# Optimization experiments

Measured on AMD Instinct MI355X. Metric: run time of the kernel, lower is better.

The kernel has to match this reference:

```python
import jax, jax.numpy as jnp
import numpy as np

B, N, C, H = 4, 2048, 1024, 16
D = C // H  # head_dim = 64
SCALE = D ** -0.5


def setup_inputs() -> dict:
    key = jax.random.key(0)
    ks = jax.random.split(key, 7)
    # freqs_cis = exp(i*theta): unit-modulus rotations, as in standard RoPE
    theta = jax.random.uniform(ks[1], (B, N, D // 2), jnp.float32, 0.0, 2 * np.pi)
    return {
        "x": jax.random.normal(ks[0], (B, N, C), jnp.float32),
        "freqs_cos": jnp.cos(theta),
        "freqs_sin": jnp.sin(theta),
        "attn_mask": jax.random.normal(ks[2], (1, 1, N, N), jnp.float32) * 0.1,
        "Wqkv": jax.random.normal(ks[3], (3 * C, C), jnp.float32) * (C ** -0.5),
        "Wproj": jax.random.normal(ks[4], (C, C), jnp.float32) * (C ** -0.5),
        "bproj": jnp.zeros((C,), jnp.float32),
    }


def _rope(t, cos, sin):
    # t: [B,H,N,D]; cos/sin: [B,1,N,D/2]; complex multiply on interleaved pairs
    tr = t.reshape(*t.shape[:-1], D // 2, 2)
    t0, t1 = tr[..., 0], tr[..., 1]
    out = jnp.stack([t0 * cos - t1 * sin, t0 * sin + t1 * cos], axis=-1)
    return out.reshape(t.shape)


def reference(x, freqs_cos, freqs_sin, attn_mask, Wqkv, Wproj, bproj):
    qkv = x @ Wqkv.T  # [B,N,3C]
    qkv = qkv.reshape(B, N, 3, H, D).transpose(2, 0, 3, 1, 4)  # [3,B,H,N,D]
    q, k, v = qkv[0], qkv[1], qkv[2]
    cos = freqs_cos[:, None]  # [B,1,N,D/2]
    sin = freqs_sin[:, None]
    q = _rope(q, cos, sin)
    k = _rope(k, cos, sin)
    attn = jnp.einsum("bhnd,bhmd->bhnm", q * SCALE, k) + attn_mask
    attn = jax.nn.softmax(attn, axis=-1)
    out = jnp.einsum("bhnm,bhmd->bhnd", attn, v)  # [B,H,N,D]
    out = out.transpose(0, 2, 1, 3).reshape(B, N, C)
    return out @ Wproj.T + bproj
```

## Files before the change

kernel.cpp:

```cpp
#include <hip/hip_runtime.h>
#include <hip/hip_bf16.h>
#include <stdint.h>


typedef __bf16 bf16;
typedef __bf16 bf16x4 __attribute__((ext_vector_type(4)));
typedef __bf16 bf16x8 __attribute__((ext_vector_type(8)));
typedef float  f32x4  __attribute__((ext_vector_type(4)));
typedef float  f32x16 __attribute__((ext_vector_type(16)));
typedef int    int4v  __attribute__((ext_vector_type(4)));

#define MFMA16(a, b, c) __builtin_amdgcn_mfma_f32_16x16x32_bf16((a), (b), (c), 0, 0, 0)
#define MFMA32(a, b, c) __builtin_amdgcn_mfma_f32_32x32x16_bf16((a), (b), (c), 0, 0, 0)

__device__ __forceinline__ bf16x4 cvt4s(float a, float b, float c, float d) {
  bf16x4 r;
  r[0] = (bf16)a; r[1] = (bf16)b; r[2] = (bf16)c; r[3] = (bf16)d;
  return r;
}
__device__ __forceinline__ bf16x8 cvt8(f32x4 a, f32x4 b) {
  bf16x8 r;
  r[0] = (bf16)a[0]; r[1] = (bf16)a[1]; r[2] = (bf16)a[2]; r[3] = (bf16)a[3];
  r[4] = (bf16)b[0]; r[5] = (bf16)b[1]; r[6] = (bf16)b[2]; r[7] = (bf16)b[3];
  return r;
}

template<int MODE>
__global__ __launch_bounds__(256)
void gemm_bt(const void* __restrict__ Av, const float* __restrict__ B,
             void* __restrict__ O0, bf16* __restrict__ O1, bf16* __restrict__ O2,
             const float* __restrict__ bias)
{
  constexpr int K = 1024;
  __shared__ __attribute__((aligned(16))) bf16 As[128 * 64];
  __shared__ __attribute__((aligned(16))) bf16 Bs[128 * 64];
  const int tid = threadIdx.x, lane = tid & 63, wid = tid >> 6;
  const int m0 = blockIdx.x * 128, n0 = blockIdx.y * 128;
  const int wm = (wid >> 1) * 64, wn = (wid & 1) * 64;
  const int l15 = lane & 15, lg = lane >> 4;

  f32x4 acc[4][4] = {};

  for (int k0 = 0; k0 < K; k0 += 64) {
#pragma unroll
    for (int it = 0; it < 4; ++it) {
      const int e = (it * 256 + tid) * 8;
      const int row = e >> 6, col = e & 63;
      const float* bp = B + (size_t)(n0 + row) * K + k0 + col;
      *(bf16x8*)(Bs + row * 64 + col) =
          cvt8(*(const f32x4*)bp, *(const f32x4*)(bp + 4));
    }
    if (MODE == 0) {
      const float* A = (const float*)Av;
#pragma unroll
      for (int it = 0; it < 4; ++it) {
        const int e = (it * 256 + tid) * 8;
        const int row = e >> 6, col = e & 63;
        const float* ap = A + (size_t)(m0 + row) * K + k0 + col;
        *(bf16x8*)(As + row * 64 + col) =
            cvt8(*(const f32x4*)ap, *(const f32x4*)(ap + 4));
      }
    } else {
      const bf16* A = (const bf16*)Av;
#pragma unroll
      for (int it = 0; it < 4; ++it) {
        const int e = (it * 256 + tid) * 8;
        const int row = e >> 6, col = e & 63;
        *(bf16x8*)(As + row * 64 + col) =
            *(const bf16x8*)(A + (size_t)(m0 + row) * K + k0 + col);
      }
    }
    __syncthreads();

    bf16x8 af[4][2], bb[4][2];
#pragma unroll
    for (int i = 0; i < 4; ++i)
#pragma unroll
      for (int kk = 0; kk < 2; ++kk) {
        af[i][kk] = *(const bf16x8*)(As + (wm + i * 16 + l15) * 64 + kk * 32 + lg * 8);
        bb[i][kk] = *(const bf16x8*)(Bs + (wn + i * 16 + l15) * 64 + kk * 32 + lg * 8);
      }
#pragma unroll
    for (int mi = 0; mi < 4; ++mi)
#pragma unroll
      for (int ni = 0; ni < 4; ++ni)
#pragma unroll
        for (int kk = 0; kk < 2; ++kk)
          acc[mi][ni] = MFMA16(af[mi][kk], bb[ni][kk], acc[mi][ni]);
    __syncthreads();
  }

#pragma unroll
  for (int mi = 0; mi < 4; ++mi)
#pragma unroll
    for (int ni = 0; ni < 4; ++ni)
#pragma unroll
      for (int r = 0; r < 4; ++r) {
        const int row = m0 + wm + mi * 16 + lg * 4 + r;
        const int col = n0 + wn + ni * 16 + l15;
        float v = acc[mi][ni][r];
        if (MODE == 0) {
          const int s = col >> 10, h = (col >> 6) & 15, d = col & 63;
          const int b = row >> 11, n = row & 2047;
          const bf16 bv = (bf16)v;
          if (s == 0)
            ((bf16*)O0)[(((size_t)(b * 16 + h) * 2048) + n) * 64 + d] = bv;
          else if (s == 1)
            O1[(((size_t)(b * 16 + h) * 2048) + n) * 64 + d] = bv;
          else
            O2[(((size_t)(b * 16 + h) * 64) + d) * 2048 + n] = bv;
        } else {
          ((float*)O0)[(size_t)row * 1024 + col] = v + bias[col];
        }
      }
}

__global__ __launch_bounds__(256)
void rope_k(bf16* __restrict__ Q, bf16* __restrict__ K,
            const float* __restrict__ C, const float* __restrict__ S)
{
  const int gid = blockIdx.x * 256 + threadIdx.x;
  const int part = gid & 3;
  const int rowid = gid >> 2;
  const int n = rowid & 2047;
  const int b = rowid >> 15;
  const size_t cbase = ((size_t)(b * 2048 + n)) * 32 + part * 8;

  float cf[8], sf[8];
  *(f32x4*)cf = *(const f32x4*)(C + cbase);
  *(f32x4*)(cf + 4) = *(const f32x4*)(C + cbase + 4);
  *(f32x4*)sf = *(const f32x4*)(S + cbase);
  *(f32x4*)(sf + 4) = *(const f32x4*)(S + cbase + 4);

  bf16* qp = Q + (size_t)rowid * 64 + part * 16;
  bf16* kp = K + (size_t)rowid * 64 + part * 16;
  __attribute__((aligned(16))) bf16 buf[16];

  *(int4v*)buf = *(const int4v*)qp;
  *(int4v*)(buf + 8) = *(const int4v*)(qp + 8);
#pragma unroll
  for (int j = 0; j < 8; ++j) {
    const float t0 = (float)buf[2 * j], t1 = (float)buf[2 * j + 1];
    buf[2 * j]     = (bf16)(t0 * cf[j] - t1 * sf[j]);
    buf[2 * j + 1] = (bf16)(t0 * sf[j] + t1 * cf[j]);
  }
  *(int4v*)qp = *(int4v*)buf;
  *(int4v*)(qp + 8) = *(int4v*)(buf + 8);

  *(int4v*)buf = *(const int4v*)kp;
  *(int4v*)(buf + 8) = *(const int4v*)(kp + 8);
#pragma unroll
  for (int j = 0; j < 8; ++j) {
    const float t0 = (float)buf[2 * j], t1 = (float)buf[2 * j + 1];
    buf[2 * j]     = (bf16)(t0 * cf[j] - t1 * sf[j]);
    buf[2 * j + 1] = (bf16)(t0 * sf[j] + t1 * cf[j]);
  }
  *(int4v*)kp = *(int4v*)buf;
  *(int4v*)(kp + 8) = *(int4v*)(buf + 8);
}

__global__ __launch_bounds__(256, 4)
void attn_k(const bf16* __restrict__ Q, const bf16* __restrict__ K,
            const bf16* __restrict__ VT, const float* __restrict__ M,
             bf16* __restrict__ O)
{
  constexpr float SCALE_LOG2E = 0.125f * 1.4426950408889634f;
  constexpr float LOG2E = 1.4426950408889634f;
  __shared__ __attribute__((aligned(16))) bf16 SH[9216];
  bf16* Kt = SH;
  bf16* Vt = SH + 4096;

  const int tid = threadIdx.x, lane = tid & 63, w = tid >> 6;
  const int bh = blockIdx.x;
  const int q0 = blockIdx.y * 128;
  const int b = bh >> 4, h = bh & 15;
  const int l31 = lane & 31, hi = lane >> 5;
  const int swz = (l31 & 7) << 3;

  const bf16* Qb = Q + (size_t)bh * 2048 * 64;
  const bf16* Kb = K + (size_t)bh * 2048 * 64;
  const bf16* Vb = VT + (size_t)bh * 64 * 2048;
  const float* Mq = M + (size_t)(q0 + w * 32 + l31) * 2048;

  bf16x8 qf[4];
  {
    const bf16* qr = Qb + (size_t)(q0 + w * 32 + l31) * 64 + 8 * hi;
#pragma unroll
    for (int j = 0; j < 4; ++j) qf[j] = *(const bf16x8*)(qr + 16 * j);
  }

  f32x16 o[2] = {{0,0,0,0,0,0,0,0,0,0,0,0,0,0,0,0},
                 {0,0,0,0,0,0,0,0,0,0,0,0,0,0,0,0}};
  float li = 0.f;

  for (int kv0 = 0; kv0 < 2048; kv0 += 64) {
#pragma unroll
    for (int it = 0; it < 2; ++it) {
      const int idx = it * 256 + tid;
      const int row = idx >> 3, g8 = (idx & 7) * 8;
      const int sc = g8 ^ ((row & 7) << 3);
      *(int4v*)(Kt + row * 64 + sc) =
          *(const int4v*)(Kb + (size_t)(kv0 + row) * 64 + g8);
      *(int4v*)(Vt + row * 64 + sc) =
          *(const int4v*)(Vb + (size_t)row * 2048 + kv0 + g8);
    }

    f32x4 mk_all[2][4];
#pragma unroll
    for (int sub = 0; sub < 2; ++sub)
#pragma unroll
      for (int rg = 0; rg < 4; ++rg)
        mk_all[sub][rg] = *(const f32x4*)(Mq + kv0 + 32 * sub + 8 * rg + 4 * hi);

    __syncthreads();

#pragma unroll
    for (int sub = 0; sub < 2; ++sub) {
      f32x16 s = {0,0,0,0,0,0,0,0,0,0,0,0,0,0,0,0};
#pragma unroll
      for (int j = 0; j < 4; ++j) {
        const bf16x8 kf = *(const bf16x8*)(
            Kt + (sub * 32 + l31) * 64 + ((16 * j + 8 * hi) ^ swz));
        s = MFMA32(kf, qf[j], s);
      }

      float rs = 0.f;
#pragma unroll
      for (int rg = 0; rg < 4; ++rg)
#pragma unroll
        for (int i = 0; i < 4; ++i) {
          const float p = __builtin_exp2f(
              fmaf(s[4 * rg + i], SCALE_LOG2E, mk_all[sub][rg][i] * LOG2E));
          s[4 * rg + i] = p;
          rs += p;
        }
      rs += __shfl_xor(rs, 32);
      li += rs;

      uint32_t pk0, pk1, pk2, pk3, pk4, pk5, pk6, pk7;
      asm("v_cvt_pk_bf16_f32 %0, %1, %2" : "=v"(pk0) : "v"(s[0]),  "v"(s[1]));
      asm("v_cvt_pk_bf16_f32 %0, %1, %2" : "=v"(pk1) : "v"(s[2]),  "v"(s[3]));
      asm("v_cvt_pk_bf16_f32 %0, %1, %2" : "=v"(pk2) : "v"(s[4]),  "v"(s[5]));
      asm("v_cvt_pk_bf16_f32 %0, %1, %2" : "=v"(pk3) : "v"(s[6]),  "v"(s[7]));
      asm("v_cvt_pk_bf16_f32 %0, %1, %2" : "=v"(pk4) : "v"(s[8]),  "v"(s[9]));
      asm("v_cvt_pk_bf16_f32 %0, %1, %2" : "=v"(pk5) : "v"(s[10]), "v"(s[11]));
      asm("v_cvt_pk_bf16_f32 %0, %1, %2" : "=v"(pk6) : "v"(s[12]), "v"(s[13]));
      asm("v_cvt_pk_bf16_f32 %0, %1, %2" : "=v"(pk7) : "v"(s[14]), "v"(s[15]));
      asm("v_permlane32_swap_b32 %0, %1" : "+v"(pk0), "+v"(pk2));
      asm("v_permlane32_swap_b32 %0, %1" : "+v"(pk1), "+v"(pk3));
      asm("v_permlane32_swap_b32 %0, %1" : "+v"(pk4), "+v"(pk6));
      asm("v_permlane32_swap_b32 %0, %1" : "+v"(pk5), "+v"(pk7));
      uint32_t pau[2][4] = {{pk0, pk1, pk2, pk3}, {pk4, pk5, pk6, pk7}};
      bf16x8 pa[2];
      __builtin_memcpy(&pa[0], pau[0], 16);
      __builtin_memcpy(&pa[1], pau[1], 16);

#pragma unroll
      for (int kh = 0; kh < 2; ++kh)
#pragma unroll
        for (int dblk = 0; dblk < 2; ++dblk) {
          const bf16x8 vf = *(const bf16x8*)(
              Vt + (dblk * 32 + l31) * 64 + ((sub * 32 + kh * 16 + 8 * hi) ^ swz));
          o[dblk] = MFMA32(vf, pa[kh], o[dblk]);
        }
    }
    __syncthreads();
  }

  const float inv = 1.f / li;
  bf16* ow = SH + w * 2304;
#pragma unroll
  for (int dblk = 0; dblk < 2; ++dblk)
#pragma unroll
    for (int rg = 0; rg < 4; ++rg)
      *(bf16x4*)(ow + l31 * 72 + dblk * 32 + 8 * rg + 4 * hi) =
          cvt4s(o[dblk][4 * rg] * inv, o[dblk][4 * rg + 1] * inv,
                o[dblk][4 * rg + 2] * inv, o[dblk][4 * rg + 3] * inv);
  asm volatile("s_waitcnt lgkmcnt(0)" ::: "memory");
  __builtin_amdgcn_sched_barrier(0);
#pragma unroll
  for (int p = 0; p < 4; ++p) {
    const int row = p * 8 + (lane >> 3);
    const int n = q0 + w * 32 + row;
    const int4v v = *(const int4v*)(ow + row * 72 + (lane & 7) * 8);
    *(int4v*)(O + ((size_t)b * 2048 + n) * 1024 + h * 64 + (lane & 7) * 8) = v;
  }
}

extern "C" void kernel_launch(void* const* d_in, const int* in_sizes, int n_in,
                              void* d_out, int out_size, void* d_ws, size_t ws_size,
                              hipStream_t stream)
{
  (void)in_sizes; (void)n_in; (void)out_size;
  const float* x     = (const float*)d_in[0];
  const float* fcos  = (const float*)d_in[1];
  const float* fsin  = (const float*)d_in[2];
  const float* mask  = (const float*)d_in[3];
  const float* wqkv  = (const float*)d_in[4];
  const float* wproj = (const float*)d_in[5];
  const float* bproj = (const float*)d_in[6];
  float* out = (float*)d_out;

  const size_t SZ = (size_t)64 * 2048 * 64 * 2;
  if (ws_size < 4 * SZ) return;
  char* ws = (char*)d_ws;
  bf16* Qr = (bf16*)(ws);
  bf16* Kr = (bf16*)(ws + SZ);
  bf16* VT = (bf16*)(ws + 2 * SZ);
  bf16* Ob = (bf16*)(ws + 3 * SZ);

  gemm_bt<0><<<dim3(64, 24), 256, 0, stream>>>(x, wqkv, Qr, Kr, VT, nullptr);
  rope_k<<<2048, 256, 0, stream>>>(Qr, Kr, fcos, fsin);
  attn_k<<<dim3(64, 16), 256, 0, stream>>>(Qr, Kr, VT, mask, Ob);
  gemm_bt<1><<<dim3(64, 8), 256, 0, stream>>>(Ob, wproj, out, nullptr, nullptr, bproj);
}
```

Before: 320.7 us.

## Pre-convert weights and mask to bf16, use direct-to-LDS loads, add MFMA priority

Adds a conversion kernel that turns Wqkv, Wproj and the attention mask (pre-scaled by log2e) into bf16 buffers in the workspace before the GEMMs and attention run. The GEMM B operand, and the A operand in the bf16 mode, are then loaded with global_load_lds straight into shared memory instead of being converted per tile in registers. Attention reads the bf16 mask, halving the mask traffic each block repeats, and wraps its MFMA sections in s_setprio. The cost is extra conversion launches and workspace use, with a fallback to the fp32 mask path when the workspace is too small.

```diff
diff --git a/kernel.cpp b/kernel.cpp
--- a/kernel.cpp
+++ b/kernel.cpp
@@ -24,10 +24,24 @@
   r[4] = (bf16)b[0]; r[5] = (bf16)b[1]; r[6] = (bf16)b[2]; r[7] = (bf16)b[3];
   return r;
 }
+__device__ __forceinline__ void gload16(const void* g, void* l) {
+  __builtin_amdgcn_global_load_lds((const __attribute__((address_space(1))) void*)g,
+                                   (__attribute__((address_space(3))) void*)l, 16, 0, 0);
+}
+
+__global__ __launch_bounds__(256)
+void cvt_k(const float* __restrict__ W, bf16* __restrict__ Wb, float scale)
+{
+  const size_t i = ((size_t)blockIdx.x * 256 + threadIdx.x) * 8;
+  const float* p = W + i;
+  f32x4 a = *(const f32x4*)p * scale;
+  f32x4 b = *(const f32x4*)(p + 4) * scale;
+  *(bf16x8*)(Wb + i) = cvt8(a, b);
+}
 
 template<int MODE>
 __global__ __launch_bounds__(256)
-void gemm_bt(const void* __restrict__ Av, const float* __restrict__ B,
+void gemm_bt(const void* __restrict__ Av, const bf16* __restrict__ B,
              void* __restrict__ O0, bf16* __restrict__ O1, bf16* __restrict__ O2,
              const float* __restrict__ bias)
 {
@@ -43,12 +57,12 @@
 
   for (int k0 = 0; k0 < K; k0 += 64) {
 #pragma unroll
-    for (int it = 0; it < 4; ++it) {
-      const int e = (it * 256 + tid) * 8;
-      const int row = e >> 6, col = e & 63;
-      const float* bp = B + (size_t)(n0 + row) * K + k0 + col;
-      *(bf16x8*)(Bs + row * 64 + col) =
-          cvt8(*(const f32x4*)bp, *(const f32x4*)(bp + 4));
+    for (int c = 0; c < 4; ++c) {
+      const int seg = wid * 4 + c;
+      const int o = seg * 1024 + lane * 16;
+      const int row = o >> 7, colb = o & 127;
+      gload16((const char*)B + (((size_t)(n0 + row) * K + k0) << 1) + colb,
+              (char*)Bs + seg * 1024);
     }
     if (MODE == 0) {
       const float* A = (const float*)Av;
@@ -63,11 +77,12 @@
     } else {
       const bf16* A = (const bf16*)Av;
 #pragma unroll
-      for (int it = 0; it < 4; ++it) {
-        const int e = (it * 256 + tid) * 8;
-        const int row = e >> 6, col = e & 63;
-        *(bf16x8*)(As + row * 64 + col) =
-            *(const bf16x8*)(A + (size_t)(m0 + row) * K + k0 + col);
+      for (int c = 0; c < 4; ++c) {
+        const int seg = wid * 4 + c;
+        const int o = seg * 1024 + lane * 16;
+        const int row = o >> 7, colb = o & 127;
+        gload16((const char*)A + (((size_t)(m0 + row) * K + k0) << 1) + colb,
+                (char*)As + seg * 1024);
       }
     }
     __syncthreads();
@@ -159,10 +174,11 @@
   *(int4v*)(kp + 8) = *(int4v*)(buf + 8);
 }
 
+template<int MM>
 __global__ __launch_bounds__(256, 4)
 void attn_k(const bf16* __restrict__ Q, const bf16* __restrict__ K,
-            const bf16* __restrict__ VT, const float* __restrict__ M,
-             bf16* __restrict__ O)
+            const bf16* __restrict__ VT, const void* __restrict__ Mv,
+            bf16* __restrict__ O)
 {
   constexpr float SCALE_LOG2E = 0.125f * 1.4426950408889634f;
   constexpr float LOG2E = 1.4426950408889634f;
@@ -180,7 +196,8 @@
   const bf16* Qb = Q + (size_t)bh * 2048 * 64;
   const bf16* Kb = K + (size_t)bh * 2048 * 64;
   const bf16* Vb = VT + (size_t)bh * 64 * 2048;
-  const float* Mq = M + (size_t)(q0 + w * 32 + l31) * 2048;
+  const float* Mqf = (const float*)Mv + (size_t)(q0 + w * 32 + l31) * 2048;
+  const bf16*  Mqb = (const bf16*)Mv  + (size_t)(q0 + w * 32 + l31) * 2048;
 
   bf16x8 qf[4];
   {
@@ -205,32 +222,40 @@
           *(const int4v*)(Vb + (size_t)row * 2048 + kv0 + g8);
     }
 
-    f32x4 mk_all[2][4];
+    f32x4 mkf[2][4];
+    bf16x4 mkb[2][4];
 #pragma unroll
     for (int sub = 0; sub < 2; ++sub)
 #pragma unroll
-      for (int rg = 0; rg < 4; ++rg)
-        mk_all[sub][rg] = *(const f32x4*)(Mq + kv0 + 32 * sub + 8 * rg + 4 * hi);
+      for (int rg = 0; rg < 4; ++rg) {
+        if (MM == 0)
+          mkf[sub][rg] = *(const f32x4*)(Mqf + kv0 + 32 * sub + 8 * rg + 4 * hi);
+        else
+          mkb[sub][rg] = *(const bf16x4*)(Mqb + kv0 + 32 * sub + 8 * rg + 4 * hi);
+      }
 
     __syncthreads();
 
 #pragma unroll
     for (int sub = 0; sub < 2; ++sub) {
       f32x16 s = {0,0,0,0,0,0,0,0,0,0,0,0,0,0,0,0};
+      __builtin_amdgcn_s_setprio(1);
 #pragma unroll
       for (int j = 0; j < 4; ++j) {
         const bf16x8 kf = *(const bf16x8*)(
             Kt + (sub * 32 + l31) * 64 + ((16 * j + 8 * hi) ^ swz));
         s = MFMA32(kf, qf[j], s);
       }
+      __builtin_amdgcn_s_setprio(0);
 
       float rs = 0.f;
 #pragma unroll
       for (int rg = 0; rg < 4; ++rg)
 #pragma unroll
         for (int i = 0; i < 4; ++i) {
-          const float p = __builtin_exp2f(
-              fmaf(s[4 * rg + i], SCALE_LOG2E, mk_all[sub][rg][i] * LOG2E));
+          const float madd = (MM == 0) ? mkf[sub][rg][i] * LOG2E
+                                       : (float)mkb[sub][rg][i];
+          const float p = __builtin_exp2f(fmaf(s[4 * rg + i], SCALE_LOG2E, madd));
           s[4 * rg + i] = p;
           rs += p;
         }
@@ -255,6 +280,7 @@
       __builtin_memcpy(&pa[0], pau[0], 16);
       __builtin_memcpy(&pa[1], pau[1], 16);
 
+      __builtin_amdgcn_s_setprio(1);
 #pragma unroll
       for (int kh = 0; kh < 2; ++kh)
 #pragma unroll
@@ -263,6 +289,7 @@
               Vt + (dblk * 32 + l31) * 64 + ((sub * 32 + kh * 16 + 8 * hi) ^ swz));
           o[dblk] = MFMA32(vf, pa[kh], o[dblk]);
         }
+      __builtin_amdgcn_s_setprio(0);
     }
     __syncthreads();
   }
@@ -301,16 +328,31 @@
   const float* bproj = (const float*)d_in[6];
   float* out = (float*)d_out;
 
-  const size_t SZ = (size_t)64 * 2048 * 64 * 2;
-  if (ws_size < 4 * SZ) return;
+  const size_t SZ  = (size_t)64 * 2048 * 64 * 2;
+  const size_t WQB = (size_t)3072 * 1024 * 2;
+  const size_t WPB = (size_t)1024 * 1024 * 2;
+  const size_t MKB = (size_t)2048 * 2048 * 2;
+  const size_t BASE = 4 * SZ + WQB + WPB;
+  if (ws_size < BASE) return;
   char* ws = (char*)d_ws;
-  bf16* Qr = (bf16*)(ws);
-  bf16* Kr = (bf16*)(ws + SZ);
-  bf16* VT = (bf16*)(ws + 2 * SZ);
-  bf16* Ob = (bf16*)(ws + 3 * SZ);
-
-  gemm_bt<0><<<dim3(64, 24), 256, 0, stream>>>(x, wqkv, Qr, Kr, VT, nullptr);
+  bf16* Qr  = (bf16*)(ws);
+  bf16* Kr  = (bf16*)(ws + SZ);
+  bf16* VT  = (bf16*)(ws + 2 * SZ);
+  bf16* Ob  = (bf16*)(ws + 3 * SZ);
+  bf16* Wqb = (bf16*)(ws + 4 * SZ);
+  bf16* Wpb = (bf16*)(ws + 4 * SZ + WQB);
+  bf16* Mb  = (bf16*)(ws + BASE);
+  const bool useMb = (ws_size >= BASE + MKB);
+  constexpr float LOG2E = 1.4426950408889634f;
+
+  cvt_k<<<1536, 256, 0, stream>>>(wqkv, Wqb, 1.0f);
+  cvt_k<<<512, 256, 0, stream>>>(wproj, Wpb, 1.0f);
+  if (useMb) cvt_k<<<2048, 256, 0, stream>>>(mask, Mb, LOG2E);
+  gemm_bt<0><<<dim3(64, 24), 256, 0, stream>>>(x, Wqb, Qr, Kr, VT, nullptr);
   rope_k<<<2048, 256, 0, stream>>>(Qr, Kr, fcos, fsin);
-  attn_k<<<dim3(64, 16), 256, 0, stream>>>(Qr, Kr, VT, mask, Ob);
-  gemm_bt<1><<<dim3(64, 8), 256, 0, stream>>>(Ob, wproj, out, nullptr, nullptr, bproj);
-}
+  if (useMb)
+    attn_k<1><<<dim3(64, 16), 256, 0, stream>>>(Qr, Kr, VT, Mb, Ob);
+  else
+    attn_k<0><<<dim3(64, 16), 256, 0, stream>>>(Qr, Kr, VT, mask, Ob);
+  gemm_bt<1><<<dim3(64, 8), 256, 0, stream>>>(Ob, Wpb, out, nullptr, nullptr, bproj);
+}
```

Measured after the change: 304.8 us. -5.0%, faster.
